# Optimization experiments

Measured on AMD Instinct MI355X. Metric: run time of the kernel, lower is better.

Reference implementation:

```python
import jax, jax.numpy as jnp
import numpy as np


def setup_inputs() -> dict:
    key = jax.random.key(0)
    k1, k2 = jax.random.split(key)
    B, C, H, W = 16, 512, 64, 64
    x = jax.random.normal(k1, (B, C, H, W), dtype=jnp.float32)
    gamma = jax.random.normal(k2, (1,), dtype=jnp.float32)
    return {"x": x, "gamma": gamma}


def reference(x, gamma):
    # x: [B, C, H, W]
    B, C, H, W = x.shape
    q = x.reshape(B, C, H * W)              # query = key = value = flattened x
    # energy[b, i, j] = <channel_i, channel_j>  -> [B, C, C]
    energy = jnp.einsum('bin,bjn->bij', q, q)
    # attention = softmax(max(energy, -1) - energy) over last dim
    logits = jnp.max(energy, axis=-1, keepdims=True) - energy
    attention = jax.nn.softmax(logits, axis=-1)
    out = jnp.einsum('bij,bjn->bin', attention, q).reshape(B, C, H, W)
    return gamma * out + x
```

## Files before the change

### kernel.cpp

```cpp
#include <hip/hip_runtime.h>
#include <hip/hip_bf16.h>
#include <cstdint>


typedef short    bf16x8 __attribute__((ext_vector_type(8)));
typedef float    f32x4  __attribute__((ext_vector_type(4)));
typedef uint16_t u16x4  __attribute__((ext_vector_type(4)));
typedef uint16_t u16x8  __attribute__((ext_vector_type(8)));

#define AS1 __attribute__((address_space(1)))
#define AS3 __attribute__((address_space(3)))

__device__ __forceinline__ void load_lds16(const void* g, void* l) {
  __builtin_amdgcn_global_load_lds((const AS1 unsigned int*)g,
                                   (AS3 unsigned int*)l, 16, 0, 0);
}

static constexpr int  BB  = 16, C = 512, N = 4096;
static constexpr long XSZ = (long)BB * C * N;
static constexpr long ESZ = (long)BB * C * C;
static constexpr int  ZSPLIT = 4;

__global__ __launch_bounds__(256) void cam_splitT(
    const float* __restrict__ x, uint16_t* __restrict__ qT) {
  __shared__ uint16_t tile[64][65];
  const int t  = threadIdx.x;
  const int b  = blockIdx.z;
  const int c0 = blockIdx.y * 64;
  const int n0 = blockIdx.x * 64;
  const float* xb  = x  + (long)b * C * N;
  uint16_t*    qTb = qT + (long)b * N * C;
  const int cl = t >> 4;
  const int nl = (t & 15) * 4;
  for (int r = 0; r < 4; ++r) {
    const int  c   = cl + r * 16;
    const long off = (long)(c0 + c) * N + n0 + nl;
    const float4 v = *(const float4*)(xb + off);
    const float vv[4] = {v.x, v.y, v.z, v.w};
    for (int k = 0; k < 4; ++k) {
      __hip_bfloat16 hb = __float2bfloat16(vv[k]);
      tile[c][nl + k] = *(uint16_t*)&hb;
    }
  }
  __syncthreads();
  for (int r = 0; r < 4; ++r) {
    const int n  = cl + r * 16;
    const int cc = (t & 15) * 4;
    u16x4 o = {tile[cc + 0][n], tile[cc + 1][n], tile[cc + 2][n], tile[cc + 3][n]};
    *(u16x4*)(qTb + (long)(n0 + n) * C + c0 + cc) = o;
  }
}

__device__ __forceinline__ void split4(float4 v, uint2& h, uint2& l) {
  const uint32_t u0 = __float_as_uint(v.x), u1 = __float_as_uint(v.y);
  const uint32_t u2 = __float_as_uint(v.z), u3 = __float_as_uint(v.w);
  const float r0 = v.x - __uint_as_float(u0 & 0xffff0000u);
  const float r1 = v.y - __uint_as_float(u1 & 0xffff0000u);
  const float r2 = v.z - __uint_as_float(u2 & 0xffff0000u);
  const float r3 = v.w - __uint_as_float(u3 & 0xffff0000u);
  h.x = (u0 >> 16) | (u1 & 0xffff0000u);
  h.y = (u2 >> 16) | (u3 & 0xffff0000u);
  l.x = (__float_as_uint(r0) >> 16) | (__float_as_uint(r1) & 0xffff0000u);
  l.y = (__float_as_uint(r2) >> 16) | (__float_as_uint(r3) & 0xffff0000u);
}

__global__ __launch_bounds__(256) void cam_energy(
    const float* __restrict__ x, float* __restrict__ E) {
  __shared__ uint16_t smem[4 * 128 * 32];
  const int tid = threadIdx.x;
  const int wave = tid >> 6, lane = tid & 63;
  const int idx = blockIdx.x;
  const int low = idx & 7, chunk = idx >> 3;
  const int gh = chunk / 10, t = chunk - gh * 10;
  const int g  = gh * 8 + low;
  const int b  = g >> 2, z = g & 3;
  const int ti = (t < 4) ? 0 : (t < 7) ? 1 : (t < 9) ? 2 : 3;
  const int tj = t - ((ti * (9 - ti)) >> 1) + ti;
  const bool diag = (ti == tj);
  const int i0 = ti * 128, j0 = tj * 128;
  const float* xb = x + (long)b * C * N;
  const int sr = tid >> 3;
  const int sc = (tid & 7) * 4;
  const float* pA = xb + (long)(i0 + sr) * N + sc;
  const float* pB = xb + (long)(j0 + sr) * N + sc;
  uint16_t* smAh = smem;
  uint16_t* smAl = smem + 4096;
  uint16_t* smBh = diag ? smem        : smem + 8192;
  uint16_t* smBl = diag ? smem + 4096 : smem + 12288;
  const int wr = wave >> 1, wc = wave & 1;
  const int m16 = lane & 15, q4 = lane >> 4;
  f32x4 acc[4][4] = {};
  const int k0 = z * (N / ZSPLIT);
  for (int kk = k0; kk < k0 + N / ZSPLIT; kk += 32) {
    for (int p = 0; p < 4; ++p) {
      const int row = p * 32 + sr;
      float4 va = *(const float4*)(pA + kk + (long)p * 32 * N);
      uint2 h, l;
      split4(va, h, l);
      *(uint2*)(smAh + row * 32 + sc) = h;
      *(uint2*)(smAl + row * 32 + sc) = l;
      if (!diag) {
        float4 vb = *(const float4*)(pB + kk + (long)p * 32 * N);
        split4(vb, h, l);
        *(uint2*)(smem + 8192 + row * 32 + sc) = h;
        *(uint2*)(smem + 12288 + row * 32 + sc) = l;
      }
    }
    __syncthreads();
    bf16x8 ah[4], al[4], bh[4], bl[4];
    for (int i = 0; i < 4; ++i) {
      const int r = wr * 64 + i * 16 + m16;
      ah[i] = *(const bf16x8*)(smAh + r * 32 + q4 * 8);
      al[i] = *(const bf16x8*)(smAl + r * 32 + q4 * 8);
    }
    for (int j = 0; j < 4; ++j) {
      const int r = wc * 64 + j * 16 + m16;
      bh[j] = *(const bf16x8*)(smBh + r * 32 + q4 * 8);
      bl[j] = *(const bf16x8*)(smBl + r * 32 + q4 * 8);
    }
    for (int i = 0; i < 4; ++i)
      for (int j = 0; j < 4; ++j) {
        acc[i][j] = __builtin_amdgcn_mfma_f32_16x16x32_bf16(ah[i], bh[j], acc[i][j], 0, 0, 0);
        acc[i][j] = __builtin_amdgcn_mfma_f32_16x16x32_bf16(ah[i], bl[j], acc[i][j], 0, 0, 0);
        acc[i][j] = __builtin_amdgcn_mfma_f32_16x16x32_bf16(al[i], bh[j], acc[i][j], 0, 0, 0);
      }
    __syncthreads();
  }
  float* Eb = E + (long)z * ESZ + (long)b * C * C;
  for (int i = 0; i < 4; ++i) {
    const int rb = i0 + wr * 64 + i * 16 + q4 * 4;
    for (int j = 0; j < 4; ++j) {
      const int cc = j0 + wc * 64 + j * 16 + m16;
      for (int r = 0; r < 4; ++r)
        Eb[(long)(rb + r) * C + cc] = acc[i][j][r];
      if (!diag)
        *(f32x4*)(Eb + (long)cc * C + rb) = acc[i][j];
    }
  }
}

__global__ __launch_bounds__(256) void cam_softmax(
    const float* __restrict__ E, uint16_t* __restrict__ attn) {
  const int t = threadIdx.x;
  const int wave = t >> 6, lane = t & 63;
  const long row = (long)blockIdx.x * 4 + wave;
  const float* e = E + row * C + lane * 8;
  float vv[8] = {};
  for (int z = 0; z < ZSPLIT; ++z) {
    const float4 a0 = *(const float4*)(e + (long)z * ESZ);
    const float4 a1 = *(const float4*)(e + (long)z * ESZ + 4);
    vv[0] += a0.x; vv[1] += a0.y; vv[2] += a0.z; vv[3] += a0.w;
    vv[4] += a1.x; vv[5] += a1.y; vv[6] += a1.z; vv[7] += a1.w;
  }
  float m = vv[0];
  for (int k = 1; k < 8; ++k) m = fminf(m, vv[k]);
  for (int s = 32; s; s >>= 1) m = fminf(m, __shfl_xor(m, s));
  float w[8], sum = 0.f;
  for (int k = 0; k < 8; ++k) { w[k] = __expf(m - vv[k]); sum += w[k]; }
  for (int s = 32; s; s >>= 1) sum += __shfl_xor(sum, s);
  const float inv = 1.0f / sum;
  u16x8 o;
  for (int k = 0; k < 8; ++k) {
    __hip_bfloat16 h = __float2bfloat16(w[k] * inv);
    o[k] = *(uint16_t*)&h;
  }
  *(u16x8*)(attn + row * C + lane * 8) = o;
}

__global__ __launch_bounds__(256) void cam_pv(
    const uint16_t* __restrict__ attn, const uint16_t* __restrict__ qT,
    const float* __restrict__ x, const float* __restrict__ gamma,
    float* __restrict__ out) {
  __shared__ uint16_t smem[2 * 128 * 32];
  const int t = threadIdx.x;
  const int wave = t >> 6, lane = t & 63;
  const int b  = blockIdx.z;
  const int i0 = blockIdx.y * 128;
  const int n0 = blockIdx.x * 128;
  const uint16_t* Ab = attn + (long)b * C * C;
  const uint16_t* Tb = qT   + (long)b * N * C;
  const int lrow = lane >> 2, lk8 = (lane & 3) * 8;
  const int wr = wave >> 1, wc = wave & 1;
  const int m16 = lane & 15, q4 = lane >> 4;
  f32x4 acc[4][4] = {};
  for (int kk = 0; kk < C; kk += 32) {
    for (int s = 0; s < 2; ++s) {
      const int row = (s * 4 + wave) * 16 + lrow;
      const uint32_t loff = (uint32_t)(s * 4 + wave) * 1024;
      char* lp = (char*)smem + loff;
      load_lds16(Ab + (long)(i0 + row) * C + kk + lk8, lp);
      load_lds16(Tb + (long)(n0 + row) * C + kk + lk8, lp + 8192);
    }
    __syncthreads();
    bf16x8 a[4], bb[4];
    for (int i = 0; i < 4; ++i)
      a[i]  = *(const bf16x8*)(smem +        (wr * 64 + i * 16 + m16) * 32 + q4 * 8);
    for (int j = 0; j < 4; ++j)
      bb[j] = *(const bf16x8*)(smem + 4096 + (wc * 64 + j * 16 + m16) * 32 + q4 * 8);
    for (int i = 0; i < 4; ++i)
      for (int j = 0; j < 4; ++j)
        acc[i][j] = __builtin_amdgcn_mfma_f32_16x16x32_bf16(a[i], bb[j], acc[i][j], 0, 0, 0);
    __syncthreads();
  }
  const float g = gamma[0];
  const float* xb = x   + (long)b * C * N;
  float*       ob = out + (long)b * C * N;
  for (int i = 0; i < 4; ++i) {
    const int rb = i0 + wr * 64 + i * 16 + q4 * 4;
    for (int j = 0; j < 4; ++j) {
      const int cc = n0 + wc * 64 + j * 16 + m16;
      for (int r = 0; r < 4; ++r) {
        const long idx = (long)(rb + r) * N + cc;
        ob[idx] = g * acc[i][j][r] + xb[idx];
      }
    }
  }
}

extern "C" void kernel_launch(void* const* d_in, const int* in_sizes, int n_in,
                              void* d_out, int out_size, void* d_ws, size_t ws_size,
                              hipStream_t stream) {
  const float* x     = (const float*)d_in[0];
  const float* gamma = (const float*)d_in[1];
  float* out = (float*)d_out;
  char*  ws  = (char*)d_ws;
  uint16_t* qT   = (uint16_t*)ws;
  float*    E    = (float*)  (ws + XSZ * 2);
  uint16_t* attn = (uint16_t*)(ws + XSZ * 2 + (long)ZSPLIT * ESZ * 4);

  cam_splitT <<<dim3(N / 64, C / 64, BB), 256, 0, stream>>>(x, qT);
  cam_energy <<<dim3(640),                256, 0, stream>>>(x, E);
  cam_softmax<<<dim3((BB * C) / 4),       256, 0, stream>>>(E, attn);
  cam_pv     <<<dim3(N / 128, C / 128, BB), 256, 0, stream>>>(attn, qT, x, gamma, out);
}
```

Baseline: 450.0 us.

## Prefetch energy tiles into registers, double split-K, widen PV K-tile, vectorize transpose

The energy kernel now loads the next K-slab of fp32 inputs into registers while the current slab is split into bf16 hi/lo parts and multiplied, overlapping global loads with MFMA work. ZSPLIT grows from 4 to 8, doubling the energy grid to 1280 blocks for better occupancy, at the cost of more partial energy matrices written and then summed in softmax. The PV kernel stages a 64-wide K tile per barrier instead of 32, halving the number of synchronizations. The transpose kernel packs its bf16 writes into vector LDS stores with a padded row stride.

Result: faster. 414.7 us (-7.8%).

```diff
diff --git a/kernel.cpp b/kernel.cpp
--- a/kernel.cpp
+++ b/kernel.cpp
@@ -19,11 +19,11 @@
 static constexpr int  BB  = 16, C = 512, N = 4096;
 static constexpr long XSZ = (long)BB * C * N;
 static constexpr long ESZ = (long)BB * C * C;
-static constexpr int  ZSPLIT = 4;
+static constexpr int  ZSPLIT = 8;
 
 __global__ __launch_bounds__(256) void cam_splitT(
     const float* __restrict__ x, uint16_t* __restrict__ qT) {
-  __shared__ uint16_t tile[64][65];
+  __shared__ uint16_t tile[64][68];
   const int t  = threadIdx.x;
   const int b  = blockIdx.z;
   const int c0 = blockIdx.y * 64;
@@ -37,10 +37,12 @@
     const long off = (long)(c0 + c) * N + n0 + nl;
     const float4 v = *(const float4*)(xb + off);
     const float vv[4] = {v.x, v.y, v.z, v.w};
+    u16x4 hv;
     for (int k = 0; k < 4; ++k) {
       __hip_bfloat16 hb = __float2bfloat16(vv[k]);
-      tile[c][nl + k] = *(uint16_t*)&hb;
-    }
+      hv[k] = *(uint16_t*)&hb;
+    }
+    *(u16x4*)&tile[c][nl] = hv;
   }
   __syncthreads();
   for (int r = 0; r < 4; ++r) {
@@ -73,7 +75,7 @@
   const int low = idx & 7, chunk = idx >> 3;
   const int gh = chunk / 10, t = chunk - gh * 10;
   const int g  = gh * 8 + low;
-  const int b  = g >> 2, z = g & 3;
+  const int b  = g >> 3, z = g & 7;
   const int ti = (t < 4) ? 0 : (t < 7) ? 1 : (t < 9) ? 2 : 3;
   const int tj = t - ((ti * (9 - ti)) >> 1) + ti;
   const bool diag = (ti == tj);
@@ -90,23 +92,34 @@
   const int wr = wave >> 1, wc = wave & 1;
   const int m16 = lane & 15, q4 = lane >> 4;
   f32x4 acc[4][4] = {};
-  const int k0 = z * (N / ZSPLIT);
-  for (int kk = k0; kk < k0 + N / ZSPLIT; kk += 32) {
+  const int k0 = z * (N / ZSPLIT), kend = k0 + N / ZSPLIT;
+  float4 ra[4], rb[4];
+  #pragma unroll
+  for (int p = 0; p < 4; ++p) {
+    ra[p] = *(const float4*)(pA + k0 + (long)p * 32 * N);
+    if (!diag) rb[p] = *(const float4*)(pB + k0 + (long)p * 32 * N);
+  }
+  for (int kk = k0; kk < kend; kk += 32) {
+    #pragma unroll
     for (int p = 0; p < 4; ++p) {
       const int row = p * 32 + sr;
-      float4 va = *(const float4*)(pA + kk + (long)p * 32 * N);
       uint2 h, l;
-      split4(va, h, l);
+      split4(ra[p], h, l);
       *(uint2*)(smAh + row * 32 + sc) = h;
       *(uint2*)(smAl + row * 32 + sc) = l;
       if (!diag) {
-        float4 vb = *(const float4*)(pB + kk + (long)p * 32 * N);
-        split4(vb, h, l);
+        split4(rb[p], h, l);
         *(uint2*)(smem + 8192 + row * 32 + sc) = h;
         *(uint2*)(smem + 12288 + row * 32 + sc) = l;
       }
     }
     __syncthreads();
+    const int kn = (kk + 32 < kend) ? kk + 32 : k0;
+    #pragma unroll
+    for (int p = 0; p < 4; ++p) {
+      ra[p] = *(const float4*)(pA + kn + (long)p * 32 * N);
+      if (!diag) rb[p] = *(const float4*)(pB + kn + (long)p * 32 * N);
+    }
     bf16x8 ah[4], al[4], bh[4], bl[4];
     for (int i = 0; i < 4; ++i) {
       const int r = wr * 64 + i * 16 + m16;
@@ -128,13 +141,13 @@
   }
   float* Eb = E + (long)z * ESZ + (long)b * C * C;
   for (int i = 0; i < 4; ++i) {
-    const int rb = i0 + wr * 64 + i * 16 + q4 * 4;
+    const int rb_ = i0 + wr * 64 + i * 16 + q4 * 4;
     for (int j = 0; j < 4; ++j) {
       const int cc = j0 + wc * 64 + j * 16 + m16;
       for (int r = 0; r < 4; ++r)
-        Eb[(long)(rb + r) * C + cc] = acc[i][j][r];
+        Eb[(long)(rb_ + r) * C + cc] = acc[i][j][r];
       if (!diag)
-        *(f32x4*)(Eb + (long)cc * C + rb) = acc[i][j];
+        *(f32x4*)(Eb + (long)cc * C + rb_) = acc[i][j];
     }
   }
 }
@@ -171,7 +184,7 @@
     const uint16_t* __restrict__ attn, const uint16_t* __restrict__ qT,
     const float* __restrict__ x, const float* __restrict__ gamma,
     float* __restrict__ out) {
-  __shared__ uint16_t smem[2 * 128 * 32];
+  __shared__ uint16_t smem[2 * 128 * 64];
   const int t = threadIdx.x;
   const int wave = t >> 6, lane = t & 63;
   const int b  = blockIdx.z;
@@ -179,27 +192,30 @@
   const int n0 = blockIdx.x * 128;
   const uint16_t* Ab = attn + (long)b * C * C;
   const uint16_t* Tb = qT   + (long)b * N * C;
-  const int lrow = lane >> 2, lk8 = (lane & 3) * 8;
+  const int lrow8 = lane >> 3;
+  const int lk8   = (lane & 7) * 8;
   const int wr = wave >> 1, wc = wave & 1;
   const int m16 = lane & 15, q4 = lane >> 4;
   f32x4 acc[4][4] = {};
-  for (int kk = 0; kk < C; kk += 32) {
-    for (int s = 0; s < 2; ++s) {
-      const int row = (s * 4 + wave) * 16 + lrow;
+  for (int kk = 0; kk < C; kk += 64) {
+    for (int s = 0; s < 4; ++s) {
+      const int row = (s * 4 + wave) * 8 + lrow8;
       const uint32_t loff = (uint32_t)(s * 4 + wave) * 1024;
       char* lp = (char*)smem + loff;
       load_lds16(Ab + (long)(i0 + row) * C + kk + lk8, lp);
-      load_lds16(Tb + (long)(n0 + row) * C + kk + lk8, lp + 8192);
-    }
-    __syncthreads();
-    bf16x8 a[4], bb[4];
-    for (int i = 0; i < 4; ++i)
-      a[i]  = *(const bf16x8*)(smem +        (wr * 64 + i * 16 + m16) * 32 + q4 * 8);
-    for (int j = 0; j < 4; ++j)
-      bb[j] = *(const bf16x8*)(smem + 4096 + (wc * 64 + j * 16 + m16) * 32 + q4 * 8);
-    for (int i = 0; i < 4; ++i)
+      load_lds16(Tb + (long)(n0 + row) * C + kk + lk8, lp + 16384);
+    }
+    __syncthreads();
+    for (int h = 0; h < 2; ++h) {
+      bf16x8 a[4], bb[4];
+      for (int i = 0; i < 4; ++i)
+        a[i]  = *(const bf16x8*)(smem +        (wr * 64 + i * 16 + m16) * 64 + h * 32 + q4 * 8);
       for (int j = 0; j < 4; ++j)
-        acc[i][j] = __builtin_amdgcn_mfma_f32_16x16x32_bf16(a[i], bb[j], acc[i][j], 0, 0, 0);
+        bb[j] = *(const bf16x8*)(smem + 8192 + (wc * 64 + j * 16 + m16) * 64 + h * 32 + q4 * 8);
+      for (int i = 0; i < 4; ++i)
+        for (int j = 0; j < 4; ++j)
+          acc[i][j] = __builtin_amdgcn_mfma_f32_16x16x32_bf16(a[i], bb[j], acc[i][j], 0, 0, 0);
+    }
     __syncthreads();
   }
   const float g = gamma[0];
@@ -229,7 +245,7 @@
   uint16_t* attn = (uint16_t*)(ws + XSZ * 2 + (long)ZSPLIT * ESZ * 4);
 
   cam_splitT <<<dim3(N / 64, C / 64, BB), 256, 0, stream>>>(x, qT);
-  cam_energy <<<dim3(640),                256, 0, stream>>>(x, E);
+  cam_energy <<<dim3(1280),               256, 0, stream>>>(x, E);
   cam_softmax<<<dim3((BB * C) / 4),       256, 0, stream>>>(E, attn);
   cam_pv     <<<dim3(N / 128, C / 128, BB), 256, 0, stream>>>(attn, qT, x, gamma, out);
 }
```
